# Optimization experiments

Hardware: AMD Instinct MI355X
Metric: run time of the kernel (lower is better)

The kernel has to match this reference:

```python
import jax, jax.numpy as jnp
import numpy as np

B, N = 8192, 2048
_EPS = 1e-5


def setup_inputs() -> dict:
    key = jax.random.key(0)
    k1, k2, k3 = jax.random.split(key, 3)
    src = jax.random.normal(k1, (B, 3, N), dtype=jnp.float32)
    src_corr = jax.random.normal(k2, (B, 3, N), dtype=jnp.float32)
    weights = jax.random.uniform(k3, (B, N), dtype=jnp.float32)
    return {"src": src, "src_corr": src_corr, "weights": weights}


def reference(src, src_corr, weights):
    # src, src_corr: (B, 3, N); weights: (B, N)
    a = jnp.swapaxes(src, -1, -2)        # (B, N, 3)
    b = jnp.swapaxes(src_corr, -1, -2)   # (B, N, 3)
    w = weights[..., None]               # (B, N, 1)
    wn = w / (jnp.sum(w, axis=1, keepdims=True) + _EPS)
    centroid_a = jnp.sum(a * wn, axis=1)  # (B, 3)
    centroid_b = jnp.sum(b * wn, axis=1)  # (B, 3)
    a_c = a - centroid_a[:, None, :]
    b_c = b - centroid_b[:, None, :]
    # cov = a_c^T @ (b_c * wn) -> (B, 3, 3)
    cov = jnp.einsum('bnd,bne->bde', a_c, b_c * wn)
    u, s, vh = jnp.linalg.svd(cov, full_matrices=False)
    v = jnp.swapaxes(vh, -1, -2)
    ut = jnp.swapaxes(u, -1, -2)
    rot_pos = v @ ut
    v_neg = v.at[:, :, 2].multiply(-1.0)  # flip last column of v
    rot_neg = v_neg @ ut
    rot = jnp.where(jnp.linalg.det(rot_pos)[:, None, None] > 0, rot_pos, rot_neg)
    translation = centroid_b - jnp.einsum('bij,bj->bi', rot, centroid_a)  # (B, 3)
    return rot, translation
```

## Files before the change

### kernel.cpp

```cpp
#include <hip/hip_runtime.h>
#include <math.h>


constexpr int kB = 8192;
constexpr int kN = 2048;
constexpr float kEps = 1e-5f;

__global__ __launch_bounds__(512) void wproc_reduce(
    const float* __restrict__ src,
    const float* __restrict__ src_corr,
    const float* __restrict__ weights,
    float* __restrict__ ws)
{
    const int b = blockIdx.x;
    const int tid = threadIdx.x;
    const float* arow = src + (size_t)b * 3 * kN;
    const float* brow = src_corr + (size_t)b * 3 * kN;

    const float4 w  = reinterpret_cast<const float4*>(weights + (size_t)b * kN)[tid];
    const float4 ax = reinterpret_cast<const float4*>(arow)[tid];
    const float4 ay = reinterpret_cast<const float4*>(arow + kN)[tid];
    const float4 az = reinterpret_cast<const float4*>(arow + 2 * kN)[tid];
    const float4 bx = reinterpret_cast<const float4*>(brow)[tid];
    const float4 by = reinterpret_cast<const float4*>(brow + kN)[tid];
    const float4 bz = reinterpret_cast<const float4*>(brow + 2 * kN)[tid];

    float acc[16];
    {
        const float wc[4]  = {w.x,  w.y,  w.z,  w.w};
        const float axc[4] = {ax.x, ax.y, ax.z, ax.w};
        const float ayc[4] = {ay.x, ay.y, ay.z, ay.w};
        const float azc[4] = {az.x, az.y, az.z, az.w};
        const float bxc[4] = {bx.x, bx.y, bx.z, bx.w};
        const float byc[4] = {by.x, by.y, by.z, by.w};
        const float bzc[4] = {bz.x, bz.y, bz.z, bz.w};
#pragma unroll
        for (int i = 0; i < 16; ++i) acc[i] = 0.f;
#pragma unroll
        for (int c = 0; c < 4; ++c) {
            const float ww  = wc[c];
            const float wax = ww * axc[c], way = ww * ayc[c], waz = ww * azc[c];
            const float bxx = bxc[c], byy = byc[c], bzz = bzc[c];
            acc[0]  += ww;
            acc[1]  += wax;       acc[2]  += way;       acc[3]  += waz;
            acc[4]  += ww * bxx;  acc[5]  += ww * byy;  acc[6]  += ww * bzz;
            acc[7]  += wax * bxx; acc[8]  += wax * byy; acc[9]  += wax * bzz;
            acc[10] += way * bxx; acc[11] += way * byy; acc[12] += way * bzz;
            acc[13] += waz * bxx; acc[14] += waz * byy; acc[15] += waz * bzz;
        }
    }

#pragma unroll
    for (int i = 0; i < 16; ++i) {
        float v = acc[i];
#pragma unroll
        for (int off = 32; off > 0; off >>= 1)
            v += __shfl_down(v, off, 64);
        acc[i] = v;
    }

    __shared__ float red[8][16];
    const int lane = tid & 63;
    const int wid  = tid >> 6;
    if (lane == 0) {
#pragma unroll
        for (int i = 0; i < 16; ++i) red[wid][i] = acc[i];
    }
    __syncthreads();
    if (tid < 16) {
        float s = 0.f;
#pragma unroll
        for (int k = 0; k < 8; ++k) s += red[k][tid];
        ws[(size_t)b * 16 + tid] = s;
    }
}

__global__ __launch_bounds__(256) void wproc_solve(
    const float* __restrict__ ws,
    float* __restrict__ out)
{
    const int b = blockIdx.x * blockDim.x + threadIdx.x;
    if (b >= kB) return;

    float t[16];
#pragma unroll
    for (int i = 0; i < 4; ++i) {
        const float4 v = reinterpret_cast<const float4*>(ws + (size_t)b * 16)[i];
        t[4 * i] = v.x; t[4 * i + 1] = v.y; t[4 * i + 2] = v.z; t[4 * i + 3] = v.w;
    }

    const float W   = t[0];
    const float inv = 1.f / (W + kEps);
    const float S   = W * inv;
    float ca[3], cb[3];
#pragma unroll
    for (int d = 0; d < 3; ++d) { ca[d] = t[1 + d] * inv; cb[d] = t[4 + d] * inv; }

    float M[3][3];
    const float f2 = 2.f - S;
#pragma unroll
    for (int d = 0; d < 3; ++d)
#pragma unroll
        for (int e = 0; e < 3; ++e)
            M[d][e] = t[7 + 3 * d + e] * inv - ca[d] * cb[e] * f2;

    const float T  = M[0][0] + M[1][1] + M[2][2];
    const float cx = M[1][2] - M[2][1];
    const float cy = M[2][0] - M[0][2];
    const float cz = M[0][1] - M[1][0];
    float Nm[4][4];
    Nm[0][0] = T;
    Nm[0][1] = Nm[1][0] = cx;
    Nm[0][2] = Nm[2][0] = cy;
    Nm[0][3] = Nm[3][0] = cz;
    Nm[1][1] = 2.f * M[0][0] - T;
    Nm[2][2] = 2.f * M[1][1] - T;
    Nm[3][3] = 2.f * M[2][2] - T;
    Nm[1][2] = Nm[2][1] = M[0][1] + M[1][0];
    Nm[1][3] = Nm[3][1] = M[0][2] + M[2][0];
    Nm[2][3] = Nm[3][2] = M[1][2] + M[2][1];

    float Vv[4][4] = {{1,0,0,0},{0,1,0,0},{0,0,1,0},{0,0,0,1}};
    const int pp[6] = {0,0,0,1,1,2};
    const int qq[6] = {1,2,3,2,3,3};
    for (int sweep = 0; sweep < 6; ++sweep) {
        for (int r = 0; r < 6; ++r) {
            const int p = pp[r], q = qq[r];
            const float apq = Nm[p][q];
            if (fabsf(apq) < 1e-12f) continue;
            const float tau = (Nm[q][q] - Nm[p][p]) / (2.f * apq);
            const float tt  = copysignf(1.f, tau) / (fabsf(tau) + sqrtf(1.f + tau * tau));
            const float c   = 1.f / sqrtf(1.f + tt * tt);
            const float s   = tt * c;
            const float app = Nm[p][p], aqq = Nm[q][q];
            Nm[p][p] = app - tt * apq;
            Nm[q][q] = aqq + tt * apq;
            Nm[p][q] = Nm[q][p] = 0.f;
#pragma unroll
            for (int k = 0; k < 4; ++k) {
                if (k == p || k == q) continue;
                const float akp = Nm[k][p], akq = Nm[k][q];
                Nm[k][p] = Nm[p][k] = c * akp - s * akq;
                Nm[k][q] = Nm[q][k] = s * akp + c * akq;
            }
#pragma unroll
            for (int k = 0; k < 4; ++k) {
                const float vkp = Vv[k][p], vkq = Vv[k][q];
                Vv[k][p] = c * vkp - s * vkq;
                Vv[k][q] = s * vkp + c * vkq;
            }
        }
    }

    int jm = 0;
#pragma unroll
    for (int j = 1; j < 4; ++j) if (Nm[j][j] > Nm[jm][jm]) jm = j;
    float qw = Vv[0][jm], qx = Vv[1][jm], qy = Vv[2][jm], qz = Vv[3][jm];
    const float nq = 1.f / sqrtf(qw * qw + qx * qx + qy * qy + qz * qz);
    qw *= nq; qx *= nq; qy *= nq; qz *= nq;

    float R[3][3];
    R[0][0] = 1.f - 2.f * (qy * qy + qz * qz);
    R[0][1] = 2.f * (qx * qy - qw * qz);
    R[0][2] = 2.f * (qx * qz + qw * qy);
    R[1][0] = 2.f * (qx * qy + qw * qz);
    R[1][1] = 1.f - 2.f * (qx * qx + qz * qz);
    R[1][2] = 2.f * (qy * qz - qw * qx);
    R[2][0] = 2.f * (qx * qz - qw * qy);
    R[2][1] = 2.f * (qy * qz + qw * qx);
    R[2][2] = 1.f - 2.f * (qx * qx + qy * qy);

    float* ro = out + (size_t)b * 9;
#pragma unroll
    for (int i = 0; i < 3; ++i)
#pragma unroll
        for (int j = 0; j < 3; ++j)
            ro[3 * i + j] = R[i][j];

    float* to = out + (size_t)kB * 9 + (size_t)b * 3;
#pragma unroll
    for (int i = 0; i < 3; ++i)
        to[i] = cb[i] - (R[i][0] * ca[0] + R[i][1] * ca[1] + R[i][2] * ca[2]);
}

extern "C" void kernel_launch(void* const* d_in, const int* in_sizes, int n_in,
                              void* d_out, int out_size, void* d_ws, size_t ws_size,
                              hipStream_t stream) {
    const float* src      = (const float*)d_in[0];
    const float* src_corr = (const float*)d_in[1];
    const float* weights  = (const float*)d_in[2];
    float* out = (float*)d_out;
    float* ws  = (float*)d_ws;
    wproc_reduce<<<kB, 512, 0, stream>>>(src, src_corr, weights, ws);
    wproc_solve<<<(kB + 255) / 256, 256, 0, stream>>>(ws, out);
}
```

Measured before the change: 456.3 us.

## Assign one wavefront per batch row and drop the shared-memory block reduction

```diff
diff --git a/kernel.cpp b/kernel.cpp
--- a/kernel.cpp
+++ b/kernel.cpp
@@ -5,28 +5,42 @@
 constexpr int kB = 8192;
 constexpr int kN = 2048;
 constexpr float kEps = 1e-5f;
-
-__global__ __launch_bounds__(512) void wproc_reduce(
+constexpr int kWavesPerBlock = 4;
+
+__global__ __launch_bounds__(256) void wproc_reduce(
     const float* __restrict__ src,
     const float* __restrict__ src_corr,
     const float* __restrict__ weights,
     float* __restrict__ ws)
 {
-    const int b = blockIdx.x;
-    const int tid = threadIdx.x;
+    const int lane = threadIdx.x & 63;
+    const int wave = threadIdx.x >> 6;
+    const int b = blockIdx.x * kWavesPerBlock + wave;
+
     const float* arow = src + (size_t)b * 3 * kN;
     const float* brow = src_corr + (size_t)b * 3 * kN;
-
-    const float4 w  = reinterpret_cast<const float4*>(weights + (size_t)b * kN)[tid];
-    const float4 ax = reinterpret_cast<const float4*>(arow)[tid];
-    const float4 ay = reinterpret_cast<const float4*>(arow + kN)[tid];
-    const float4 az = reinterpret_cast<const float4*>(arow + 2 * kN)[tid];
-    const float4 bx = reinterpret_cast<const float4*>(brow)[tid];
-    const float4 by = reinterpret_cast<const float4*>(brow + kN)[tid];
-    const float4 bz = reinterpret_cast<const float4*>(brow + 2 * kN)[tid];
+    const float4* w4  = reinterpret_cast<const float4*>(weights + (size_t)b * kN);
+    const float4* ax4 = reinterpret_cast<const float4*>(arow);
+    const float4* ay4 = reinterpret_cast<const float4*>(arow + kN);
+    const float4* az4 = reinterpret_cast<const float4*>(arow + 2 * kN);
+    const float4* bx4 = reinterpret_cast<const float4*>(brow);
+    const float4* by4 = reinterpret_cast<const float4*>(brow + kN);
+    const float4* bz4 = reinterpret_cast<const float4*>(brow + 2 * kN);
 
     float acc[16];
-    {
+#pragma unroll
+    for (int i = 0; i < 16; ++i) acc[i] = 0.f;
+
+#pragma unroll 4
+    for (int it = 0; it < kN / 4 / 64; ++it) {
+        const int idx = it * 64 + lane;
+        const float4 w  = w4[idx];
+        const float4 ax = ax4[idx];
+        const float4 ay = ay4[idx];
+        const float4 az = az4[idx];
+        const float4 bx = bx4[idx];
+        const float4 by = by4[idx];
+        const float4 bz = bz4[idx];
         const float wc[4]  = {w.x,  w.y,  w.z,  w.w};
         const float axc[4] = {ax.x, ax.y, ax.z, ax.w};
         const float ayc[4] = {ay.x, ay.y, ay.z, ay.w};
@@ -35,18 +49,16 @@
         const float byc[4] = {by.x, by.y, by.z, by.w};
         const float bzc[4] = {bz.x, bz.y, bz.z, bz.w};
 #pragma unroll
-        for (int i = 0; i < 16; ++i) acc[i] = 0.f;
-#pragma unroll
         for (int c = 0; c < 4; ++c) {
             const float ww  = wc[c];
             const float wax = ww * axc[c], way = ww * ayc[c], waz = ww * azc[c];
             const float bxx = bxc[c], byy = byc[c], bzz = bzc[c];
             acc[0]  += ww;
-            acc[1]  += wax;       acc[2]  += way;       acc[3]  += waz;
-            acc[4]  += ww * bxx;  acc[5]  += ww * byy;  acc[6]  += ww * bzz;
-            acc[7]  += wax * bxx; acc[8]  += wax * byy; acc[9]  += wax * bzz;
-            acc[10] += way * bxx; acc[11] += way * byy; acc[12] += way * bzz;
-            acc[13] += waz * bxx; acc[14] += waz * byy; acc[15] += waz * bzz;
+            acc[1]  += wax;                acc[2]  += way;                acc[3]  += waz;
+            acc[4]  = fmaf(ww,  bxx, acc[4]);  acc[5]  = fmaf(ww,  byy, acc[5]);  acc[6]  = fmaf(ww,  bzz, acc[6]);
+            acc[7]  = fmaf(wax, bxx, acc[7]);  acc[8]  = fmaf(wax, byy, acc[8]);  acc[9]  = fmaf(wax, bzz, acc[9]);
+            acc[10] = fmaf(way, bxx, acc[10]); acc[11] = fmaf(way, byy, acc[11]); acc[12] = fmaf(way, bzz, acc[12]);
+            acc[13] = fmaf(waz, bxx, acc[13]); acc[14] = fmaf(waz, byy, acc[14]); acc[15] = fmaf(waz, bzz, acc[15]);
         }
     }
 
@@ -59,19 +71,12 @@
         acc[i] = v;
     }
 
-    __shared__ float red[8][16];
-    const int lane = tid & 63;
-    const int wid  = tid >> 6;
     if (lane == 0) {
-#pragma unroll
-        for (int i = 0; i < 16; ++i) red[wid][i] = acc[i];
-    }
-    __syncthreads();
-    if (tid < 16) {
-        float s = 0.f;
-#pragma unroll
-        for (int k = 0; k < 8; ++k) s += red[k][tid];
-        ws[(size_t)b * 16 + tid] = s;
+        float4* o = reinterpret_cast<float4*>(ws + (size_t)b * 16);
+        o[0] = make_float4(acc[0],  acc[1],  acc[2],  acc[3]);
+        o[1] = make_float4(acc[4],  acc[5],  acc[6],  acc[7]);
+        o[2] = make_float4(acc[8],  acc[9],  acc[10], acc[11]);
+        o[3] = make_float4(acc[12], acc[13], acc[14], acc[15]);
     }
 }
 
@@ -191,6 +196,6 @@
     const float* weights  = (const float*)d_in[2];
     float* out = (float*)d_out;
     float* ws  = (float*)d_ws;
-    wproc_reduce<<<kB, 512, 0, stream>>>(src, src_corr, weights, ws);
+    wproc_reduce<<<kB / kWavesPerBlock, 64 * kWavesPerBlock, 0, stream>>>(src, src_corr, weights, ws);
     wproc_solve<<<(kB + 255) / 256, 256, 0, stream>>>(ws, out);
 }
```

Result: faster. 440.9 us (-3.4%).
